# Performance work log

Hardware: AMD Instinct MI355X
Metric: run time of the kernel (lower is better)

## Reference

```python
import jax, jax.numpy as jnp
import numpy as np

N_HEAD = 8
D_MODEL = 512
D_QKV = 64
LN_EPS = 1e-6


def setup_inputs() -> dict:
    key = jax.random.key(0)
    ks = jax.random.split(key, 10)
    B, S = 4, 2048
    q = jax.random.normal(ks[0], (B, S, D_MODEL), dtype=jnp.float32)
    k = jax.random.normal(ks[1], (B, S, D_MODEL), dtype=jnp.float32)
    v = jax.random.normal(ks[2], (B, S, D_MODEL), dtype=jnp.float32)
    mask = jax.random.randint(ks[3], (B, S, S), 0, 2, dtype=jnp.int32)
    scale = 1.0 / np.sqrt(D_MODEL)
    Wq = jax.random.normal(ks[4], (D_MODEL, N_HEAD * D_QKV), dtype=jnp.float32) * scale
    Wk = jax.random.normal(ks[5], (D_MODEL, N_HEAD * D_QKV), dtype=jnp.float32) * scale
    Wv = jax.random.normal(ks[6], (D_MODEL, N_HEAD * D_QKV), dtype=jnp.float32) * scale
    Wfc = jax.random.normal(ks[7], (N_HEAD * D_QKV, D_MODEL), dtype=jnp.float32) * scale
    gamma = jnp.ones((D_MODEL,), dtype=jnp.float32)
    beta = jnp.zeros((D_MODEL,), dtype=jnp.float32)
    return {"q": q, "k": k, "v": v, "mask": mask, "Wq": Wq, "Wk": Wk,
            "Wv": Wv, "Wfc": Wfc, "gamma": gamma, "beta": beta}


def _layer_norm(x, gamma, beta):
    mu = jnp.mean(x, axis=-1, keepdims=True)
    var = jnp.mean(jnp.square(x - mu), axis=-1, keepdims=True)
    return (x - mu) * jax.lax.rsqrt(var + LN_EPS) * gamma + beta


def reference(q, k, v, mask, Wq, Wk, Wv, Wfc, gamma, beta):
    B, Sq, _ = q.shape
    Sk = k.shape[1]
    residual = q
    qn = _layer_norm(q, gamma, beta)
    # projections -> [B, S, H, Dk]
    qh = (qn @ Wq).reshape(B, Sq, N_HEAD, D_QKV)
    kh = (k @ Wk).reshape(B, Sk, N_HEAD, D_QKV)
    vh = (v @ Wv).reshape(B, Sk, N_HEAD, D_QKV)
    temp = jnp.float32(D_QKV ** 0.5)
    # scores: [B, H, Sq, Sk]
    attn = jnp.einsum('bqhd,bkhd->bhqk', qh / temp, kh)
    attn = jnp.where(mask[:, None, :, :] == 0, jnp.float32(-1e9), attn)
    attn = jax.nn.softmax(attn, axis=-1)
    out = jnp.einsum('bhqk,bkhd->bqhd', attn, vh).reshape(B, Sq, N_HEAD * D_QKV)
    out = out @ Wfc
    return out + residual
```

## Files before the change

kernel.cpp:

```cpp
#include <hip/hip_runtime.h>

#define BATCH 4
#define SEQ   2048
#define NHEAD 8
#define DQKV  64
#define DMODEL 512
#define ROWS  (BATCH*SEQ)
#define BH    (BATCH*NHEAD)
#define HSTRIDE (SEQ*DQKV)

using f32x4  = __attribute__((ext_vector_type(4))) float;
using short8 = __attribute__((ext_vector_type(8))) short;
using short4v = __attribute__((ext_vector_type(4))) short;

#define MFMA16(a,b,c) __builtin_amdgcn_mfma_f32_16x16x32_bf16((a),(b),(c),0,0,0)

__device__ __forceinline__ short f2bf(float f) {
    unsigned u = __float_as_uint(f);
    u += 0x7FFFu + ((u >> 16) & 1u);
    return (short)(u >> 16);
}

__device__ __forceinline__ void gl2lds16(const short* g, short* l) {
    __builtin_amdgcn_global_load_lds(
        (__attribute__((address_space(1))) void*)g,
        (__attribute__((address_space(3))) void*)l, 16, 0, 0);
}

__device__ __forceinline__ void stage64x64(const short* g0, int gstride, short* lt, int t) {
    #pragma unroll
    for (int p = 0; p < 2; ++p) {
        int o = p * 2048 + t * 8;
        int row = o >> 6;
        int c = ((o >> 3) & 7) ^ (row & 7);
        gl2lds16(g0 + (size_t)row * gstride + c * 8, lt + o);
    }
}
__device__ __forceinline__ void stage128x64(const short* g0, int gstride, short* lt, int t) {
    stage64x64(g0, gstride, lt, t);
    stage64x64(g0 + (size_t)64 * gstride, gstride, lt + 4096, t);
}

__device__ __forceinline__ short8 trd(const short* t, int row, int c) {
    return *(const short8*)(t + row * 64 + ((c ^ (row & 7)) << 3));
}

__global__ __launch_bounds__(256) void prep_kernel(
        const float* __restrict__ q, const float* __restrict__ k,
        const float* __restrict__ v, const float* __restrict__ gamma,
        const float* __restrict__ beta,
        short* __restrict__ qn, short* __restrict__ kb, short* __restrict__ vb) {
    if (blockIdx.y == 0) {
        int wave = threadIdx.x >> 6, lane = threadIdx.x & 63;
        int row  = blockIdx.x * 4 + wave;
        const float4* qr = (const float4*)(q + (size_t)row * DMODEL);
        float4 x0 = qr[lane * 2];
        float4 x1 = qr[lane * 2 + 1];
        float s  = x0.x + x0.y + x0.z + x0.w + x1.x + x1.y + x1.z + x1.w;
        float s2 = x0.x*x0.x + x0.y*x0.y + x0.z*x0.z + x0.w*x0.w
                 + x1.x*x1.x + x1.y*x1.y + x1.z*x1.z + x1.w*x1.w;
        #pragma unroll
        for (int m = 1; m < 64; m <<= 1) {
            s  += __shfl_xor(s,  m);
            s2 += __shfl_xor(s2, m);
        }
        float mu  = s * (1.0f / DMODEL);
        float var = s2 * (1.0f / DMODEL) - mu * mu;
        float rstd = rsqrtf(var + 1e-6f);
        const float4* g = (const float4*)gamma;
        const float4* be = (const float4*)beta;
        float4 g0 = g[lane*2], g1 = g[lane*2+1];
        float4 b0 = be[lane*2], b1 = be[lane*2+1];
        short8 o;
        o[0] = f2bf((x0.x - mu) * rstd * g0.x + b0.x);
        o[1] = f2bf((x0.y - mu) * rstd * g0.y + b0.y);
        o[2] = f2bf((x0.z - mu) * rstd * g0.z + b0.z);
        o[3] = f2bf((x0.w - mu) * rstd * g0.w + b0.w);
        o[4] = f2bf((x1.x - mu) * rstd * g1.x + b1.x);
        o[5] = f2bf((x1.y - mu) * rstd * g1.y + b1.y);
        o[6] = f2bf((x1.z - mu) * rstd * g1.z + b1.z);
        o[7] = f2bf((x1.w - mu) * rstd * g1.w + b1.w);
        ((short8*)(qn + (size_t)row * DMODEL))[lane] = o;
    } else {
        const float* src = (blockIdx.y == 1) ? k : v;
        short* dst = (blockIdx.y == 1) ? kb : vb;
        size_t i = (size_t)blockIdx.x * 2048 + (size_t)threadIdx.x * 8;
        float4 a = *(const float4*)(src + i);
        float4 b = *(const float4*)(src + i + 4);
        short8 o;
        o[0]=f2bf(a.x); o[1]=f2bf(a.y); o[2]=f2bf(a.z); o[3]=f2bf(a.w);
        o[4]=f2bf(b.x); o[5]=f2bf(b.y); o[6]=f2bf(b.z); o[7]=f2bf(b.w);
        *(short8*)(dst + i) = o;
    }
}

__global__ __launch_bounds__(256) void castWT4_kernel(
        const float* __restrict__ W0, const float* __restrict__ W1,
        const float* __restrict__ W2, const float* __restrict__ W3,
        short* __restrict__ T0, short* __restrict__ T1,
        short* __restrict__ T2, short* __restrict__ T3) {
    __shared__ short tile[64 * 68];
    int w = blockIdx.z;
    const float* W = w==0 ? W0 : w==1 ? W1 : w==2 ? W2 : W3;
    short* T = w==0 ? T0 : w==1 ? T1 : w==2 ? T2 : T3;
    int ti = blockIdx.x, tj = blockIdx.y;
    int tid = threadIdx.x;
    #pragma unroll
    for (int p = 0; p < 4; ++p) {
        int idx = tid + p * 256;
        int kl = idx >> 4, c4 = idx & 15;
        float4 f = *(const float4*)(W + (size_t)(tj*64 + kl) * DMODEL + ti*64 + c4*4);
        short4v s; s[0]=f2bf(f.x); s[1]=f2bf(f.y); s[2]=f2bf(f.z); s[3]=f2bf(f.w);
        *(short4v*)(tile + kl*68 + c4*4) = s;
    }
    __syncthreads();
    #pragma unroll
    for (int p = 0; p < 4; ++p) {
        int idx = tid + p * 256;
        int nl = idx >> 4, kseg = idx & 15;
        short4v s;
        #pragma unroll
        for (int i = 0; i < 4; ++i) s[i] = tile[(kseg*4 + i)*68 + nl];
        *(short4v*)(T + (size_t)(ti*64 + nl) * DMODEL + tj*64 + kseg*4) = s;
    }
}

__global__ __launch_bounds__(256) void maskpack_kernel(
        const int* __restrict__ mask, unsigned long long* __restrict__ mp) {
    int gw = blockIdx.x * 4 + (threadIdx.x >> 6);
    int lane = threadIdx.x & 63;
    int lm = lane & 15, lg = lane >> 4;
    int w64 = gw & 31;
    int Qg  = (gw >> 5) & 127;
    int b   = gw >> 12;
    const int* src = mask + ((size_t)b * SEQ + Qg * 16 + lm) * SEQ + w64 * 64 + lg * 4;
    unsigned long long* d = mp + (size_t)gw * 16;
    #pragma unroll
    for (int kg = 0; kg < 4; ++kg) {
        int4 v = *(const int4*)(src + kg * 16);
        unsigned long long w0 = __ballot(v.x != 0);
        unsigned long long w1 = __ballot(v.y != 0);
        unsigned long long w2 = __ballot(v.z != 0);
        unsigned long long w3 = __ballot(v.w != 0);
        if (lane == 0) {
            *(ulonglong2*)(d + kg*4)     = make_ulonglong2(w0, w1);
            *(ulonglong2*)(d + kg*4 + 2) = make_ulonglong2(w2, w3);
        }
    }
}

__global__ __launch_bounds__(256, 4) void proj_qkv_kernel(
        const short* __restrict__ qn, const short* __restrict__ kb,
        const short* __restrict__ vb,
        const short* __restrict__ Wqt, const short* __restrict__ Wkt,
        const short* __restrict__ Wvt,
        short* __restrict__ qhp, short* __restrict__ khp, short* __restrict__ vtp) {
    __shared__ __align__(16) short Wl[2 * 8192];
    int tid = threadIdx.x, wave = tid >> 6, lane = tid & 63;
    int lm = lane & 15, lg = lane >> 4;
    int which = blockIdx.y >> 2;
    int CB0 = (blockIdx.y & 3) * 128;
    const short* A  = which==0 ? qn  : which==1 ? kb  : vb;
    const short* Wt = which==0 ? Wqt : which==1 ? Wkt : Wvt;
    float scale = which==0 ? 0.18033688f : 1.0f;

    int RBw = blockIdx.x * 128 + wave * 32;
    const short* Arow0 = A + (size_t)(RBw + lm) * DMODEL;
    const short* Arow1 = A + (size_t)(RBw + 16 + lm) * DMODEL;
    const short* W0 = Wt + (size_t)CB0 * DMODEL;

    short8 a[2][2];
    a[0][0] = *(const short8*)(Arow0 + lg * 8);
    a[0][1] = *(const short8*)(Arow0 + 32 + lg * 8);
    a[1][0] = *(const short8*)(Arow1 + lg * 8);
    a[1][1] = *(const short8*)(Arow1 + 32 + lg * 8);
    stage128x64(W0, DMODEL, Wl, tid);
    __syncthreads();

    f32x4 acc[2][8] = {};
    for (int kk = 0; kk < DMODEL; kk += 64) {
        int cur = (kk >> 6) & 1;
        bool more = (kk + 64) < DMODEL;
        short8 an[2][2];
        if (more) {
            stage128x64(W0 + kk + 64, DMODEL, Wl + (cur ^ 1) * 8192, tid);
            an[0][0] = *(const short8*)(Arow0 + kk + 64 + lg * 8);
            an[0][1] = *(const short8*)(Arow0 + kk + 96 + lg * 8);
            an[1][0] = *(const short8*)(Arow1 + kk + 64 + lg * 8);
            an[1][1] = *(const short8*)(Arow1 + kk + 96 + lg * 8);
        }
        const short* Wc = Wl + cur * 8192;
        #pragma unroll
        for (int cg = 0; cg < 8; ++cg) {
            short8 b0 = trd(Wc, cg*16 + lm, lg);
            short8 b1 = trd(Wc, cg*16 + lm, lg + 4);
            #pragma unroll
            for (int rg = 0; rg < 2; ++rg) {
                acc[rg][cg] = MFMA16(a[rg][0], b0, acc[rg][cg]);
                acc[rg][cg] = MFMA16(a[rg][1], b1, acc[rg][cg]);
            }
        }
        if (more) {
            #pragma unroll
            for (int rg = 0; rg < 2; ++rg) { a[rg][0] = an[rg][0]; a[rg][1] = an[rg][1]; }
        }
        __syncthreads();
    }

    if (which < 2) {
        short* outh = which==0 ? qhp : khp;
        #pragma unroll
        for (int rg = 0; rg < 2; ++rg) {
            #pragma unroll
            for (int cg = 0; cg < 8; ++cg) {
                int n = CB0 + cg * 16 + lm;
                int h = n >> 6, d = n & 63;
                #pragma unroll
                for (int r = 0; r < 4; ++r) {
                    int m = RBw + rg * 16 + lg * 4 + r;
                    int bb = m >> 11, s = m & 2047;
                    outh[(size_t)(bb * NHEAD + h) * HSTRIDE + (size_t)s * DQKV + d] =
                        f2bf(acc[rg][cg][r] * scale);
                }
            }
        }
    } else {
        int bb = RBw >> 11;
        #pragma unroll
        for (int rg = 0; rg < 2; ++rg) {
            int s0 = (RBw + rg * 16 + lg * 4) & 2047;
            int s6 = s0 & 63;
            int pos = (s0 & ~63) | (s6 & 32) | ((s6 & 12) << 1) | ((s6 & 16) >> 2);
            #pragma unroll
            for (int cg = 0; cg < 8; ++cg) {
                int n = CB0 + cg * 16 + lm;
                int h = n >> 6, d = n & 63;
                short4v pk;
                #pragma unroll
                for (int r = 0; r < 4; ++r) pk[r] = f2bf(acc[rg][cg][r]);
                *(short4v*)(vtp + (size_t)(bb * NHEAD + h) * HSTRIDE
                            + (size_t)d * SEQ + pos) = pk;
            }
        }
    }
}

__global__ __launch_bounds__(256, 2) void attn_kernel(
        const short* __restrict__ qh, const short* __restrict__ kh,
        const short* __restrict__ vt, const unsigned long long* __restrict__ mpack,
        short* __restrict__ oh) {
    __shared__ __align__(16) short lds[16384];
    int tid = threadIdx.x, wave = tid >> 6, lane = tid & 63;
    int lm = lane & 15, lg = lane >> 4;

    int bid = blockIdx.y * gridDim.x + blockIdx.x;
    int slot = bid >> 3;
    int bh = (bid & 7) * 4 + (slot >> 4);
    int qt = slot & 15;
    int b = bh >> 3;
    int qbase = qt * 128 + wave * 32;

    const short* Kbase = kh + (size_t)bh * HSTRIDE;
    const short* Vtb   = vt + (size_t)bh * HSTRIDE;

    const short8* Qrow = (const short8*)(qh + (size_t)bh * HSTRIDE
                          + (size_t)(qbase + lm) * DQKV);
    short8 aq[2][2];
    aq[0][0] = Qrow[lg];       aq[0][1] = Qrow[lg + 4];
    aq[1][0] = Qrow[128 + lg]; aq[1][1] = Qrow[128 + lg + 4];

    int mb = __builtin_amdgcn_readfirstlane((b * 128 + qt * 8 + wave * 2) * 512);
    const unsigned long long* mbase = mpack + mb;

    const short one = (short)0x3F80;
    short8 ones8 = {one, one, one, one, one, one, one, one};

    f32x4 o[2][4] = {};
    f32x4 ox[2] = {};

    stage64x64(Kbase, DQKV, lds, tid);
    stage64x64(Vtb,   SEQ,  lds + 8192, tid);
    __syncthreads();

    for (int kt = 0; kt < SEQ; kt += 64) {
        int cur = (kt >> 6) & 1;
        if (kt + 64 < SEQ) {
            int nxt = cur ^ 1;
            stage64x64(Kbase + (size_t)(kt + 64) * DQKV, DQKV, lds + nxt * 4096, tid);
            stage64x64(Vtb + kt + 64, SEQ, lds + 8192 + nxt * 4096, tid);
        }
        const short* Kc = lds + cur * 4096;
        const short* Vc = lds + 8192 + cur * 4096;
        const unsigned long long* mw = mbase + (kt >> 6) * 16;

        f32x4 sk[2][4];
        #pragma unroll
        for (int kg = 0; kg < 4; ++kg) {
            short8 ak0 = trd(Kc, kg * 16 + lm, lg);
            short8 ak1 = trd(Kc, kg * 16 + lm, lg + 4);
            #pragma unroll
            for (int qg = 0; qg < 2; ++qg) {
                f32x4 z{};
                z = MFMA16(ak0, aq[qg][0], z);
                sk[qg][kg] = MFMA16(ak1, aq[qg][1], z);
            }
        }

        short8 pa8[2][2];
        #pragma unroll
        for (int qg = 0; qg < 2; ++qg) {
            #pragma unroll
            for (int kgp = 0; kgp < 2; ++kgp) {
                float p[8];
                #pragma unroll
                for (int jj = 0; jj < 8; ++jj) {
                    int kg = kgp * 2 + (jj >> 2), r = jj & 3;
                    unsigned long long mword = mw[qg * 512 + kg * 4 + r];
                    float e = __builtin_amdgcn_exp2f(sk[qg][kg][r]);
                    asm("v_cndmask_b32 %0, 0, %1, %2" : "=v"(p[jj]) : "v"(e), "s"(mword));
                }
                int w0, w1, w2, w3;
                asm("v_cvt_pk_bf16_f32 %0, %1, %2" : "=v"(w0) : "v"(p[0]), "v"(p[1]));
                asm("v_cvt_pk_bf16_f32 %0, %1, %2" : "=v"(w1) : "v"(p[2]), "v"(p[3]));
                asm("v_cvt_pk_bf16_f32 %0, %1, %2" : "=v"(w2) : "v"(p[4]), "v"(p[5]));
                asm("v_cvt_pk_bf16_f32 %0, %1, %2" : "=v"(w3) : "v"(p[6]), "v"(p[7]));
                union { int wi[4]; short8 s; } u;
                u.wi[0] = w0; u.wi[1] = w1; u.wi[2] = w2; u.wi[3] = w3;
                pa8[qg][kgp] = u.s;
            }
        }

        #pragma unroll
        for (int dt = 0; dt < 4; ++dt) {
            #pragma unroll
            for (int kgp = 0; kgp < 2; ++kgp) {
                short8 bv = trd(Vc, dt * 16 + lm, kgp * 4 + lg);
                o[0][dt] = MFMA16(pa8[0][kgp], bv, o[0][dt]);
                o[1][dt] = MFMA16(pa8[1][kgp], bv, o[1][dt]);
            }
        }
        #pragma unroll
        for (int qg = 0; qg < 2; ++qg) {
            ox[qg] = MFMA16(pa8[qg][0], ones8, ox[qg]);
            ox[qg] = MFMA16(pa8[qg][1], ones8, ox[qg]);
        }
        __syncthreads();
    }

    short* ob = oh + (size_t)bh * HSTRIDE;
    #pragma unroll
    for (int qg = 0; qg < 2; ++qg) {
        float rinv[4];
        #pragma unroll
        for (int r = 0; r < 4; ++r) rinv[r] = __builtin_amdgcn_rcpf(ox[qg][r]);
        #pragma unroll
        for (int dt = 0; dt < 4; ++dt) {
            #pragma unroll
            for (int r = 0; r < 4; ++r) {
                ob[(size_t)(qbase + qg * 16 + lg * 4 + r) * DQKV + dt * 16 + lm] =
                    f2bf(o[qg][dt][r] * rinv[r]);
            }
        }
    }
}

__global__ __launch_bounds__(256, 4) void outproj_kernel(
        const short* __restrict__ Ah, const short* __restrict__ Wfct,
        const float* __restrict__ resid, float* __restrict__ out) {
    __shared__ __align__(16) short Wl[2 * 4096];
    int tid = threadIdx.x, wave = tid >> 6, lane = tid & 63;
    int lm = lane & 15, lg = lane >> 4;
    int CB0 = blockIdx.y * 64;
    int RB = blockIdx.x * 64 + wave * 16;
    const short* W0 = Wfct + (size_t)CB0 * DMODEL;

    int m0 = RB + lm;
    size_t rb = (size_t)(m0 >> 11) * (NHEAD * HSTRIDE) + (size_t)(m0 & 2047) * DQKV;

    short8 a0 = *(const short8*)(Ah + rb + lg * 8);
    short8 a1 = *(const short8*)(Ah + rb + 32 + lg * 8);
    stage64x64(W0, DMODEL, Wl, tid);
    __syncthreads();

    f32x4 acc[4] = {};
    for (int kk = 0; kk < DMODEL; kk += 64) {
        int cur = (kk >> 6) & 1;
        bool more = (kk + 64) < DMODEL;
        short8 a0n, a1n;
        if (more) {
            stage64x64(W0 + kk + 64, DMODEL, Wl + (cur ^ 1) * 4096, tid);
            size_t hoff = (size_t)((kk >> 6) + 1) * HSTRIDE;
            a0n = *(const short8*)(Ah + rb + hoff + lg * 8);
            a1n = *(const short8*)(Ah + rb + hoff + 32 + lg * 8);
        }
        const short* Wc = Wl + cur * 4096;
        #pragma unroll
        for (int cg = 0; cg < 4; ++cg) {
            short8 b0 = trd(Wc, cg*16 + lm, lg);
            short8 b1 = trd(Wc, cg*16 + lm, lg + 4);
            acc[cg] = MFMA16(a0, b0, acc[cg]);
            acc[cg] = MFMA16(a1, b1, acc[cg]);
        }
        if (more) { a0 = a0n; a1 = a1n; }
        __syncthreads();
    }

    #pragma unroll
    for (int cg = 0; cg < 4; ++cg) {
        int n = CB0 + cg * 16 + lm;
        #pragma unroll
        for (int r = 0; r < 4; ++r) {
            int m = RB + lg * 4 + r;
            size_t idx = (size_t)m * DMODEL + n;
            out[idx] = acc[cg][r] + resid[idx];
        }
    }
}

extern "C" void kernel_launch(void* const* d_in, const int* in_sizes, int n_in,
                              void* d_out, int out_size, void* d_ws, size_t ws_size,
                              hipStream_t stream) {
    const float* q     = (const float*)d_in[0];
    const float* k     = (const float*)d_in[1];
    const float* v     = (const float*)d_in[2];
    const int*   mask  = (const int*)d_in[3];
    const float* Wq    = (const float*)d_in[4];
    const float* Wk    = (const float*)d_in[5];
    const float* Wv    = (const float*)d_in[6];
    const float* Wfc   = (const float*)d_in[7];
    const float* gamma = (const float*)d_in[8];
    const float* beta  = (const float*)d_in[9];
    float* out = (float*)d_out;

    char* ws = (char*)d_ws;
    const size_t SZ_ROWS = (size_t)ROWS * DMODEL * sizeof(short);
    const size_t SZ_W    = (size_t)DMODEL * DMODEL * sizeof(short);
    short* qn   = (short*)(ws);
    short* kbf  = (short*)(ws + SZ_ROWS);
    short* vbf  = (short*)(ws + 2 * SZ_ROWS);
    short* Wqt  = (short*)(ws + 3 * SZ_ROWS);
    short* Wkt  = (short*)(ws + 3 * SZ_ROWS + SZ_W);
    short* Wvt  = (short*)(ws + 3 * SZ_ROWS + 2 * SZ_W);
    short* Wfct = (short*)(ws + 3 * SZ_ROWS + 3 * SZ_W);
    short* qhb  = (short*)(ws + 3 * SZ_ROWS + 4 * SZ_W);
    short* khb  = (short*)(ws + 4 * SZ_ROWS + 4 * SZ_W);
    short* vtb  = (short*)(ws + 5 * SZ_ROWS + 4 * SZ_W);
    unsigned long long* mpack = (unsigned long long*)(ws + 6 * SZ_ROWS + 4 * SZ_W);
    short* aout = qn;

    prep_kernel<<<dim3(ROWS / 4, 3), 256, 0, stream>>>(q, k, v, gamma, beta, qn, kbf, vbf);
    castWT4_kernel<<<dim3(8, 8, 4), 256, 0, stream>>>(Wq, Wk, Wv, Wfc, Wqt, Wkt, Wvt, Wfct);
    maskpack_kernel<<<16384 / 4, 256, 0, stream>>>(mask, mpack);

    proj_qkv_kernel<<<dim3(ROWS / 128, 12), 256, 0, stream>>>(
        qn, kbf, vbf, Wqt, Wkt, Wvt, qhb, khb, vtb);

    attn_kernel<<<dim3(SEQ / 128, BH), 256, 0, stream>>>(qhb, khb, vtb, mpack, aout);

    outproj_kernel<<<dim3(ROWS / 64, DMODEL / 64), 256, 0, stream>>>(aout, Wfct, q, out);
}
```

Baseline: 251.7 us.

## Fuse prep kernels, widen attention K/V tiles to 128, double outproj row tile

Three small preprocessing kernels (layernorm/cast, weight transpose-cast, mask packing) are merged into one flat-grid launch to cut launch overhead and tail gaps. The attention kernel now stages 128-key K/V tiles per iteration, doubling LDS to 64KB, so it needs half as many barriers. The output projection gives each wave 32 rows, which halves the grid and reuses each W tile from LDS for two row groups. Risks are lower occupancy from the larger LDS allocation and higher register pressure in both GEMM-like kernels.

```diff
diff --git a/kernel.cpp b/kernel.cpp
--- a/kernel.cpp
+++ b/kernel.cpp
@@ -45,14 +45,54 @@
     return *(const short8*)(t + row * 64 + ((c ^ (row & 7)) << 3));
 }
 
-__global__ __launch_bounds__(256) void prep_kernel(
+__global__ __launch_bounds__(256) void prep_all_kernel(
         const float* __restrict__ q, const float* __restrict__ k,
         const float* __restrict__ v, const float* __restrict__ gamma,
-        const float* __restrict__ beta,
-        short* __restrict__ qn, short* __restrict__ kb, short* __restrict__ vb) {
-    if (blockIdx.y == 0) {
-        int wave = threadIdx.x >> 6, lane = threadIdx.x & 63;
-        int row  = blockIdx.x * 4 + wave;
+        const float* __restrict__ beta, const int* __restrict__ mask,
+        const float* __restrict__ W0in, const float* __restrict__ W1in,
+        const float* __restrict__ W2in, const float* __restrict__ W3in,
+        short* __restrict__ qn, short* __restrict__ kb, short* __restrict__ vb,
+        unsigned long long* __restrict__ mp,
+        short* __restrict__ T0, short* __restrict__ T1,
+        short* __restrict__ T2, short* __restrict__ T3) {
+    __shared__ short tile[64 * 68];
+    int bid = blockIdx.x;
+    int tid = threadIdx.x;
+    if (bid < 4096) {
+        int gw = bid * 4 + (tid >> 6);
+        int lane = tid & 63;
+        int lm = lane & 15, lg = lane >> 4;
+        int w64 = gw & 31;
+        int Qg  = (gw >> 5) & 127;
+        int b   = gw >> 12;
+        const int* src = mask + ((size_t)b * SEQ + Qg * 16 + lm) * SEQ + w64 * 64 + lg * 4;
+        unsigned long long* d = mp + (size_t)gw * 16;
+        #pragma unroll
+        for (int kg = 0; kg < 4; ++kg) {
+            int4 vv = *(const int4*)(src + kg * 16);
+            unsigned long long w0 = __ballot(vv.x != 0);
+            unsigned long long w1 = __ballot(vv.y != 0);
+            unsigned long long w2 = __ballot(vv.z != 0);
+            unsigned long long w3 = __ballot(vv.w != 0);
+            if (lane == 0) {
+                *(ulonglong2*)(d + kg*4)     = make_ulonglong2(w0, w1);
+                *(ulonglong2*)(d + kg*4 + 2) = make_ulonglong2(w2, w3);
+            }
+        }
+    } else if (bid < 8192) {
+        int b2 = bid - 4096;
+        const float* src = (b2 < 2048) ? k : v;
+        short* dst = (b2 < 2048) ? kb : vb;
+        size_t i = (size_t)(b2 & 2047) * 2048 + (size_t)tid * 8;
+        float4 a = *(const float4*)(src + i);
+        float4 c = *(const float4*)(src + i + 4);
+        short8 o;
+        o[0]=f2bf(a.x); o[1]=f2bf(a.y); o[2]=f2bf(a.z); o[3]=f2bf(a.w);
+        o[4]=f2bf(c.x); o[5]=f2bf(c.y); o[6]=f2bf(c.z); o[7]=f2bf(c.w);
+        *(short8*)(dst + i) = o;
+    } else if (bid < 10240) {
+        int wave = tid >> 6, lane = tid & 63;
+        int row  = (bid - 8192) * 4 + wave;
         const float4* qr = (const float4*)(q + (size_t)row * DMODEL);
         float4 x0 = qr[lane * 2];
         float4 x1 = qr[lane * 2 + 1];
@@ -82,69 +122,27 @@
         o[7] = f2bf((x1.w - mu) * rstd * g1.w + b1.w);
         ((short8*)(qn + (size_t)row * DMODEL))[lane] = o;
     } else {
-        const float* src = (blockIdx.y == 1) ? k : v;
-        short* dst = (blockIdx.y == 1) ? kb : vb;
-        size_t i = (size_t)blockIdx.x * 2048 + (size_t)threadIdx.x * 8;
-        float4 a = *(const float4*)(src + i);
-        float4 b = *(const float4*)(src + i + 4);
-        short8 o;
-        o[0]=f2bf(a.x); o[1]=f2bf(a.y); o[2]=f2bf(a.z); o[3]=f2bf(a.w);
-        o[4]=f2bf(b.x); o[5]=f2bf(b.y); o[6]=f2bf(b.z); o[7]=f2bf(b.w);
-        *(short8*)(dst + i) = o;
-    }
-}
-
-__global__ __launch_bounds__(256) void castWT4_kernel(
-        const float* __restrict__ W0, const float* __restrict__ W1,
-        const float* __restrict__ W2, const float* __restrict__ W3,
-        short* __restrict__ T0, short* __restrict__ T1,
-        short* __restrict__ T2, short* __restrict__ T3) {
-    __shared__ short tile[64 * 68];
-    int w = blockIdx.z;
-    const float* W = w==0 ? W0 : w==1 ? W1 : w==2 ? W2 : W3;
-    short* T = w==0 ? T0 : w==1 ? T1 : w==2 ? T2 : T3;
-    int ti = blockIdx.x, tj = blockIdx.y;
-    int tid = threadIdx.x;
-    #pragma unroll
-    for (int p = 0; p < 4; ++p) {
-        int idx = tid + p * 256;
-        int kl = idx >> 4, c4 = idx & 15;
-        float4 f = *(const float4*)(W + (size_t)(tj*64 + kl) * DMODEL + ti*64 + c4*4);
-        short4v s; s[0]=f2bf(f.x); s[1]=f2bf(f.y); s[2]=f2bf(f.z); s[3]=f2bf(f.w);
-        *(short4v*)(tile + kl*68 + c4*4) = s;
-    }
-    __syncthreads();
-    #pragma unroll
-    for (int p = 0; p < 4; ++p) {
-        int idx = tid + p * 256;
-        int nl = idx >> 4, kseg = idx & 15;
-        short4v s;
-        #pragma unroll
-        for (int i = 0; i < 4; ++i) s[i] = tile[(kseg*4 + i)*68 + nl];
-        *(short4v*)(T + (size_t)(ti*64 + nl) * DMODEL + tj*64 + kseg*4) = s;
-    }
-}
-
-__global__ __launch_bounds__(256) void maskpack_kernel(
-        const int* __restrict__ mask, unsigned long long* __restrict__ mp) {
-    int gw = blockIdx.x * 4 + (threadIdx.x >> 6);
-    int lane = threadIdx.x & 63;
-    int lm = lane & 15, lg = lane >> 4;
-    int w64 = gw & 31;
-    int Qg  = (gw >> 5) & 127;
-    int b   = gw >> 12;
-    const int* src = mask + ((size_t)b * SEQ + Qg * 16 + lm) * SEQ + w64 * 64 + lg * 4;
-    unsigned long long* d = mp + (size_t)gw * 16;
-    #pragma unroll
-    for (int kg = 0; kg < 4; ++kg) {
-        int4 v = *(const int4*)(src + kg * 16);
-        unsigned long long w0 = __ballot(v.x != 0);
-        unsigned long long w1 = __ballot(v.y != 0);
-        unsigned long long w2 = __ballot(v.z != 0);
-        unsigned long long w3 = __ballot(v.w != 0);
-        if (lane == 0) {
-            *(ulonglong2*)(d + kg*4)     = make_ulonglong2(w0, w1);
-            *(ulonglong2*)(d + kg*4 + 2) = make_ulonglong2(w2, w3);
+        int b4 = bid - 10240;
+        int w = b4 >> 6, ti = (b4 >> 3) & 7, tj = b4 & 7;
+        const float* W = w==0 ? W0in : w==1 ? W1in : w==2 ? W2in : W3in;
+        short* T = w==0 ? T0 : w==1 ? T1 : w==2 ? T2 : T3;
+        #pragma unroll
+        for (int p = 0; p < 4; ++p) {
+            int idx = tid + p * 256;
+            int kl = idx >> 4, c4 = idx & 15;
+            float4 f = *(const float4*)(W + (size_t)(tj*64 + kl) * DMODEL + ti*64 + c4*4);
+            short4v sv; sv[0]=f2bf(f.x); sv[1]=f2bf(f.y); sv[2]=f2bf(f.z); sv[3]=f2bf(f.w);
+            *(short4v*)(tile + kl*68 + c4*4) = sv;
+        }
+        __syncthreads();
+        #pragma unroll
+        for (int p = 0; p < 4; ++p) {
+            int idx = tid + p * 256;
+            int nl = idx >> 4, kseg = idx & 15;
+            short4v sv;
+            #pragma unroll
+            for (int i = 0; i < 4; ++i) sv[i] = tile[(kseg*4 + i)*68 + nl];
+            *(short4v*)(T + (size_t)(ti*64 + nl) * DMODEL + tj*64 + kseg*4) = sv;
         }
     }
 }
@@ -249,7 +247,7 @@
         const short* __restrict__ qh, const short* __restrict__ kh,
         const short* __restrict__ vt, const unsigned long long* __restrict__ mpack,
         short* __restrict__ oh) {
-    __shared__ __align__(16) short lds[16384];
+    __shared__ __align__(16) short lds[32768];
     int tid = threadIdx.x, wave = tid >> 6, lane = tid & 63;
     int lm = lane & 15, lg = lane >> 4;
 
@@ -274,75 +272,80 @@
 
     const short one = (short)0x3F80;
     short8 ones8 = {one, one, one, one, one, one, one, one};
+    f32x4 zero4 = {0.0f, 0.0f, 0.0f, 0.0f};
 
     f32x4 o[2][4] = {};
     f32x4 ox[2] = {};
 
-    stage64x64(Kbase, DQKV, lds, tid);
-    stage64x64(Vtb,   SEQ,  lds + 8192, tid);
+    stage128x64(Kbase, DQKV, lds, tid);
+    stage64x64(Vtb,      SEQ, lds + 16384, tid);
+    stage64x64(Vtb + 64, SEQ, lds + 16384 + 4096, tid);
     __syncthreads();
 
-    for (int kt = 0; kt < SEQ; kt += 64) {
-        int cur = (kt >> 6) & 1;
-        if (kt + 64 < SEQ) {
+    for (int kt = 0; kt < SEQ; kt += 128) {
+        int cur = (kt >> 7) & 1;
+        if (kt + 128 < SEQ) {
             int nxt = cur ^ 1;
-            stage64x64(Kbase + (size_t)(kt + 64) * DQKV, DQKV, lds + nxt * 4096, tid);
-            stage64x64(Vtb + kt + 64, SEQ, lds + 8192 + nxt * 4096, tid);
-        }
-        const short* Kc = lds + cur * 4096;
-        const short* Vc = lds + 8192 + cur * 4096;
-        const unsigned long long* mw = mbase + (kt >> 6) * 16;
-
-        f32x4 sk[2][4];
-        #pragma unroll
-        for (int kg = 0; kg < 4; ++kg) {
-            short8 ak0 = trd(Kc, kg * 16 + lm, lg);
-            short8 ak1 = trd(Kc, kg * 16 + lm, lg + 4);
+            stage128x64(Kbase + (size_t)(kt + 128) * DQKV, DQKV, lds + nxt * 8192, tid);
+            stage64x64(Vtb + kt + 128, SEQ, lds + 16384 + nxt * 8192, tid);
+            stage64x64(Vtb + kt + 192, SEQ, lds + 16384 + nxt * 8192 + 4096, tid);
+        }
+        #pragma unroll
+        for (int s = 0; s < 2; ++s) {
+            const short* Kc = lds + cur * 8192 + s * 4096;
+            const short* Vc = lds + 16384 + cur * 8192 + s * 4096;
+            const unsigned long long* mw = mbase + ((kt >> 6) + s) * 16;
+
+            f32x4 sk[2][4];
+            #pragma unroll
+            for (int kg = 0; kg < 4; ++kg) {
+                short8 ak0 = trd(Kc, kg * 16 + lm, lg);
+                short8 ak1 = trd(Kc, kg * 16 + lm, lg + 4);
+                #pragma unroll
+                for (int qg = 0; qg < 2; ++qg) {
+                    f32x4 z = MFMA16(ak0, aq[qg][0], zero4);
+                    sk[qg][kg] = MFMA16(ak1, aq[qg][1], z);
+                }
+            }
+
+            short8 pa8[2][2];
             #pragma unroll
             for (int qg = 0; qg < 2; ++qg) {
-                f32x4 z{};
-                z = MFMA16(ak0, aq[qg][0], z);
-                sk[qg][kg] = MFMA16(ak1, aq[qg][1], z);
-            }
-        }
-
-        short8 pa8[2][2];
-        #pragma unroll
-        for (int qg = 0; qg < 2; ++qg) {
-            #pragma unroll
-            for (int kgp = 0; kgp < 2; ++kgp) {
-                float p[8];
                 #pragma unroll
-                for (int jj = 0; jj < 8; ++jj) {
-                    int kg = kgp * 2 + (jj >> 2), r = jj & 3;
-                    unsigned long long mword = mw[qg * 512 + kg * 4 + r];
-                    float e = __builtin_amdgcn_exp2f(sk[qg][kg][r]);
-                    asm("v_cndmask_b32 %0, 0, %1, %2" : "=v"(p[jj]) : "v"(e), "s"(mword));
+                for (int kgp = 0; kgp < 2; ++kgp) {
+                    float p[8];
+                    #pragma unroll
+                    for (int jj = 0; jj < 8; ++jj) {
+                        int kg = kgp * 2 + (jj >> 2), r = jj & 3;
+                        unsigned long long mword = mw[qg * 512 + kg * 4 + r];
+                        float e = __builtin_amdgcn_exp2f(sk[qg][kg][r]);
+                        asm("v_cndmask_b32 %0, 0, %1, %2" : "=v"(p[jj]) : "v"(e), "s"(mword));
+                    }
+                    int w0, w1, w2, w3;
+                    asm("v_cvt_pk_bf16_f32 %0, %1, %2" : "=v"(w0) : "v"(p[0]), "v"(p[1]));
+                    asm("v_cvt_pk_bf16_f32 %0, %1, %2" : "=v"(w1) : "v"(p[2]), "v"(p[3]));
+                    asm("v_cvt_pk_bf16_f32 %0, %1, %2" : "=v"(w2) : "v"(p[4]), "v"(p[5]));
+                    asm("v_cvt_pk_bf16_f32 %0, %1, %2" : "=v"(w3) : "v"(p[6]), "v"(p[7]));
+                    union { int wi[4]; short8 s8; } u;
+                    u.wi[0] = w0; u.wi[1] = w1; u.wi[2] = w2; u.wi[3] = w3;
+                    pa8[qg][kgp] = u.s8;
                 }
-                int w0, w1, w2, w3;
-                asm("v_cvt_pk_bf16_f32 %0, %1, %2" : "=v"(w0) : "v"(p[0]), "v"(p[1]));
-                asm("v_cvt_pk_bf16_f32 %0, %1, %2" : "=v"(w1) : "v"(p[2]), "v"(p[3]));
-                asm("v_cvt_pk_bf16_f32 %0, %1, %2" : "=v"(w2) : "v"(p[4]), "v"(p[5]));
-                asm("v_cvt_pk_bf16_f32 %0, %1, %2" : "=v"(w3) : "v"(p[6]), "v"(p[7]));
-                union { int wi[4]; short8 s; } u;
-                u.wi[0] = w0; u.wi[1] = w1; u.wi[2] = w2; u.wi[3] = w3;
-                pa8[qg][kgp] = u.s;
-            }
-        }
-
-        #pragma unroll
-        for (int dt = 0; dt < 4; ++dt) {
-            #pragma unroll
-            for (int kgp = 0; kgp < 2; ++kgp) {
-                short8 bv = trd(Vc, dt * 16 + lm, kgp * 4 + lg);
-                o[0][dt] = MFMA16(pa8[0][kgp], bv, o[0][dt]);
-                o[1][dt] = MFMA16(pa8[1][kgp], bv, o[1][dt]);
-            }
-        }
-        #pragma unroll
-        for (int qg = 0; qg < 2; ++qg) {
-            ox[qg] = MFMA16(pa8[qg][0], ones8, ox[qg]);
-            ox[qg] = MFMA16(pa8[qg][1], ones8, ox[qg]);
+            }
+
+            #pragma unroll
+            for (int dt = 0; dt < 4; ++dt) {
+                #pragma unroll
+                for (int kgp = 0; kgp < 2; ++kgp) {
+                    short8 bv = trd(Vc, dt * 16 + lm, kgp * 4 + lg);
+                    o[0][dt] = MFMA16(pa8[0][kgp], bv, o[0][dt]);
+                    o[1][dt] = MFMA16(pa8[1][kgp], bv, o[1][dt]);
+                }
+            }
+            #pragma unroll
+            for (int qg = 0; qg < 2; ++qg) {
+                ox[qg] = MFMA16(pa8[qg][0], ones8, ox[qg]);
+                ox[qg] = MFMA16(pa8[qg][1], ones8, ox[qg]);
+            }
         }
         __syncthreads();
     }
@@ -371,48 +374,63 @@
     int tid = threadIdx.x, wave = tid >> 6, lane = tid & 63;
     int lm = lane & 15, lg = lane >> 4;
     int CB0 = blockIdx.y * 64;
-    int RB = blockIdx.x * 64 + wave * 16;
+    int RB = blockIdx.x * 128 + wave * 32;
     const short* W0 = Wfct + (size_t)CB0 * DMODEL;
 
-    int m0 = RB + lm;
-    size_t rb = (size_t)(m0 >> 11) * (NHEAD * HSTRIDE) + (size_t)(m0 & 2047) * DQKV;
-
-    short8 a0 = *(const short8*)(Ah + rb + lg * 8);
-    short8 a1 = *(const short8*)(Ah + rb + 32 + lg * 8);
+    int m0 = RB + lm, m1 = RB + 16 + lm;
+    size_t rb0 = (size_t)(m0 >> 11) * (NHEAD * HSTRIDE) + (size_t)(m0 & 2047) * DQKV;
+    size_t rb1 = (size_t)(m1 >> 11) * (NHEAD * HSTRIDE) + (size_t)(m1 & 2047) * DQKV;
+
+    short8 a[2][2];
+    a[0][0] = *(const short8*)(Ah + rb0 + lg * 8);
+    a[0][1] = *(const short8*)(Ah + rb0 + 32 + lg * 8);
+    a[1][0] = *(const short8*)(Ah + rb1 + lg * 8);
+    a[1][1] = *(const short8*)(Ah + rb1 + 32 + lg * 8);
     stage64x64(W0, DMODEL, Wl, tid);
     __syncthreads();
 
-    f32x4 acc[4] = {};
+    f32x4 acc[2][4] = {};
     for (int kk = 0; kk < DMODEL; kk += 64) {
         int cur = (kk >> 6) & 1;
         bool more = (kk + 64) < DMODEL;
-        short8 a0n, a1n;
+        short8 an[2][2];
         if (more) {
             stage64x64(W0 + kk + 64, DMODEL, Wl + (cur ^ 1) * 4096, tid);
             size_t hoff = (size_t)((kk >> 6) + 1) * HSTRIDE;
-            a0n = *(const short8*)(Ah + rb + hoff + lg * 8);
-            a1n = *(const short8*)(Ah + rb + hoff + 32 + lg * 8);
+            an[0][0] = *(const short8*)(Ah + rb0 + hoff + lg * 8);
+            an[0][1] = *(const short8*)(Ah + rb0 + hoff + 32 + lg * 8);
+            an[1][0] = *(const short8*)(Ah + rb1 + hoff + lg * 8);
+            an[1][1] = *(const short8*)(Ah + rb1 + hoff + 32 + lg * 8);
         }
         const short* Wc = Wl + cur * 4096;
         #pragma unroll
         for (int cg = 0; cg < 4; ++cg) {
             short8 b0 = trd(Wc, cg*16 + lm, lg);
             short8 b1 = trd(Wc, cg*16 + lm, lg + 4);
-            acc[cg] = MFMA16(a0, b0, acc[cg]);
-            acc[cg] = MFMA16(a1, b1, acc[cg]);
-        }
-        if (more) { a0 = a0n; a1 = a1n; }
+            #pragma unroll
+            for (int rg = 0; rg < 2; ++rg) {
+                acc[rg][cg] = MFMA16(a[rg][0], b0, acc[rg][cg]);
+                acc[rg][cg] = MFMA16(a[rg][1], b1, acc[rg][cg]);
+            }
+        }
+        if (more) {
+            #pragma unroll
+            for (int rg = 0; rg < 2; ++rg) { a[rg][0] = an[rg][0]; a[rg][1] = an[rg][1]; }
+        }
         __syncthreads();
     }
 
     #pragma unroll
-    for (int cg = 0; cg < 4; ++cg) {
-        int n = CB0 + cg * 16 + lm;
-        #pragma unroll
-        for (int r = 0; r < 4; ++r) {
-            int m = RB + lg * 4 + r;
-            size_t idx = (size_t)m * DMODEL + n;
-            out[idx] = acc[cg][r] + resid[idx];
+    for (int rg = 0; rg < 2; ++rg) {
+        #pragma unroll
+        for (int cg = 0; cg < 4; ++cg) {
+            int n = CB0 + cg * 16 + lm;
+            #pragma unroll
+            for (int r = 0; r < 4; ++r) {
+                int m = RB + rg * 16 + lg * 4 + r;
+                size_t idx = (size_t)m * DMODEL + n;
+                out[idx] = acc[rg][cg][r] + resid[idx];
+            }
         }
     }
 }
@@ -448,14 +466,14 @@
     unsigned long long* mpack = (unsigned long long*)(ws + 6 * SZ_ROWS + 4 * SZ_W);
     short* aout = qn;
 
-    prep_kernel<<<dim3(ROWS / 4, 3), 256, 0, stream>>>(q, k, v, gamma, beta, qn, kbf, vbf);
-    castWT4_kernel<<<dim3(8, 8, 4), 256, 0, stream>>>(Wq, Wk, Wv, Wfc, Wqt, Wkt, Wvt, Wfct);
-    maskpack_kernel<<<16384 / 4, 256, 0, stream>>>(mask, mpack);
+    prep_all_kernel<<<dim3(10496), 256, 0, stream>>>(
+        q, k, v, gamma, beta, mask, Wq, Wk, Wv, Wfc,
+        qn, kbf, vbf, mpack, Wqt, Wkt, Wvt, Wfct);
 
     proj_qkv_kernel<<<dim3(ROWS / 128, 12), 256, 0, stream>>>(
         qn, kbf, vbf, Wqt, Wkt, Wvt, qhb, khb, vtb);
 
     attn_kernel<<<dim3(SEQ / 128, BH), 256, 0, stream>>>(qhb, khb, vtb, mpack, aout);
 
-    outproj_kernel<<<dim3(ROWS / 64, DMODEL / 64), 256, 0, stream>>>(aout, Wfct, q, out);
-}
+    outproj_kernel<<<dim3(ROWS / 128, DMODEL / 64), 256, 0, stream>>>(aout, Wfct, q, out);
+}
```

Result: no change. 255.2 us (+1.4%).
